# Optimization experiments

Hardware: AMD Instinct MI355X
Metric: run time of the kernel (lower is better)

The kernel has to match this reference:

```python
import jax, jax.numpy as jnp
import numpy as np

FFT_LEN = 256
WIN_LEN = 768
FRM_LEN = 128
PPF_TAP = WIN_LEN // FFT_LEN  # 6
SCALE = -256.0
GROUP_DELAY = 648  # module uses group_delay = -648
B, C, S, T = 8, 2, FFT_LEN // 2 + 1, 4096


def _make_lpf(win_len):
    # firwin(win_len, 0.5, window='hann', scale=False) equivalent
    n = np.arange(win_len, dtype=np.float64)
    w = 0.5 - 0.5 * np.cos(2.0 * np.pi * n / (win_len - 1))
    h = w * np.sinc(0.5 * (n - (win_len - 1) / 2.0))
    return jnp.asarray(h, dtype=jnp.float32)


def setup_inputs() -> dict:
    key = jax.random.key(0)
    k1, k2 = jax.random.split(key)
    spectrum_real = jax.random.normal(k1, (B, C, S, T), dtype=jnp.float32)
    spectrum_imag = jax.random.normal(k2, (B, C, S, T), dtype=jnp.float32)
    lpf_coef = _make_lpf(WIN_LEN)
    return {"spectrum_real": spectrum_real, "spectrum_imag": spectrum_imag, "lpf_coef": lpf_coef}


def reference(spectrum_real, spectrum_imag, lpf_coef):
    # spectrum: (B, C, S, T) complex; per-frame irfft over subbands
    spec = jnp.swapaxes(spectrum_real + 1j * spectrum_imag, -1, -2)  # (B,C,T,S)
    fftout = jnp.fft.irfft(spec, n=FFT_LEN, axis=-1)                 # (B,C,T,FFT_LEN)
    rev = fftout[..., ::-1]                                          # comp_in[fft_len-j-1]
    v = jnp.tile(rev, (1, 1, 1, PPF_TAP)) * lpf_coef                 # (B,C,T,WIN_LEN)
    b, c, t, _ = v.shape
    num_samples = t * FRM_LEN
    # overlap-add: frame t contributes v[t] at offset t*FRM_LEN (shifting buffer recurrence)
    idx = jnp.arange(t)[:, None] * FRM_LEN + jnp.arange(WIN_LEN)[None, :]  # (T, WIN_LEN)
    y = jnp.zeros((b, c, num_samples + WIN_LEN), dtype=v.dtype)
    y = y.at[..., idx].add(v)[..., :num_samples]
    y = y * (FRM_LEN * SCALE)
    # circular shift by group delay, then trim the wrapped tail
    y = jnp.roll(y, -GROUP_DELAY, axis=-1)[..., :-GROUP_DELAY]
    return y
```

## Files before the change

kernel.cpp:

```cpp
#include <hip/hip_runtime.h>
#include <hip/hip_bf16.h>
#include <math.h>

#define NBINS   129
#define NFFT    256
#define WINL    768
#define TFRAMES 4096
#define OUTL    523640
#define NPAIRS  (OUTL / 2)
#define SHIFT   648
#define WSEG    26
#define CHUNK   (WSEG * 128)
#define NCHUNK  ((OUTL + CHUNK - 1) / CHUNK)
#define FF      32

#define KDIM    288
#define KROW    296
#define GROW    268
#define WBYTES  (16 * 9 * 64 * 16)
#define GBYTES  ((size_t)16 * TFRAMES * 256 * 2)
#define NSTG    17

typedef __attribute__((ext_vector_type(8))) short bf16x8;
typedef __attribute__((ext_vector_type(4))) float f32x4;

static __device__ __forceinline__ ushort f2bf(float x) {
    union { float f; unsigned u; } v; v.f = x;
    unsigned r = v.u + 0x7FFFu + ((v.u >> 16) & 1u);
    return (ushort)(r >> 16);
}

__global__ void build_w_kernel(ushort* __restrict__ wp)
{
    const int gid  = blockIdx.x * 256 + threadIdx.x;
    const int lane = gid & 63;
    const int mtks = gid >> 6;
    const int ks   = mtks % 9;
    const int mt   = mtks / 9;
    const int m    = mt * 16 + (lane & 15);
    const int kb   = ks * 32 + ((lane >> 4) << 3);

    ushort o[8];
    #pragma unroll
    for (int e = 0; e < 8; ++e) {
        const int kap = kb + e;
        float val = 0.f;
        if (kap < 258) {
            const int k = kap >> 1;
            float s, c;
            sincospif((float)(k * (m + 1)) * (1.0f / 128.0f), &s, &c);
            if (kap & 1)  val = (k >= 1 && k <= 127) ? s * (2.0f / 256.0f) : 0.f;
            else          val = (k == 0 || k == 128) ? c * (1.0f / 256.0f)
                                                     : c * (2.0f / 256.0f);
        }
        o[e] = f2bf(val);
    }
    int4 pk;
    pk.x = o[0] | (o[1] << 16); pk.y = o[2] | (o[3] << 16);
    pk.z = o[4] | (o[5] << 16); pk.w = o[6] | (o[7] << 16);
    ((int4*)wp)[gid] = pk;
}

__global__ __launch_bounds__(256, 6)
void pfb_dft_kernel(const float* __restrict__ gre, const float* __restrict__ gim,
                    const ushort* __restrict__ wp, ushort* __restrict__ Gg)
{
    __shared__ ushort s_Bu[FF * KROW];

    const int t0  = blockIdx.x * FF;
    const int bc  = blockIdx.y;
    const int tid = threadIdx.x;
    const size_t specBase = (size_t)bc * NBINS * TFRAMES;

    float vr[NSTG], vi[NSTG];
    #pragma unroll
    for (int r = 0; r < NSTG; ++r) {
        const int idx = tid + r * 256;
        float a = 0.f, b = 0.f;
        if (idx < NBINS * FF) {
            const int k = idx >> 5, f = idx & 31;
            const size_t g = specBase + (size_t)k * TFRAMES + (size_t)(t0 + f);
            a = gre[g]; b = gim[g];
        }
        vr[r] = a; vi[r] = b;
    }
    #pragma unroll
    for (int r = 0; r < NSTG; ++r) {
        const int idx = tid + r * 256;
        if (idx < NBINS * FF) {
            const int k = idx >> 5, f = idx & 31;
            __hip_bfloat162 p = __float22bfloat162_rn(make_float2(vr[r], vi[r]));
            *(__hip_bfloat162*)&s_Bu[f * KROW + 2 * k] = p;
        }
    }
    for (int idx = tid; idx < FF * (KROW - 258); idx += 256) {
        const int f = idx / (KROW - 258), r = idx - f * (KROW - 258);
        s_Bu[f * KROW + 258 + r] = 0;
    }
    __syncthreads();

    const int lane = tid & 63;
    const int wid  = tid >> 6;
    const int brow = lane & 15;
    const int kgrp = (lane >> 4) << 3;

    f32x4 acc[4][2];
    #pragma unroll
    for (int mi = 0; mi < 4; ++mi)
        #pragma unroll
        for (int nt = 0; nt < 2; ++nt)
            acc[mi][nt] = (f32x4){0.f, 0.f, 0.f, 0.f};

    const ushort* wbase0 = wp + ((size_t)(wid * 4) * 9 * 64 + (size_t)lane) * 8;
    #pragma unroll
    for (int ks = 0; ks < 9; ++ks) {
        const bf16x8 b0 = *(const bf16x8*)&s_Bu[brow * KROW + ks * 32 + kgrp];
        const bf16x8 b1 = *(const bf16x8*)&s_Bu[(16 + brow) * KROW + ks * 32 + kgrp];
        #pragma unroll
        for (int mi = 0; mi < 4; ++mi) {
            const bf16x8 aw = *(const bf16x8*)(wbase0 + mi * 4608 + ks * 512);
            acc[mi][0] = __builtin_amdgcn_mfma_f32_16x16x32_bf16(aw, b0, acc[mi][0], 0, 0, 0);
            acc[mi][1] = __builtin_amdgcn_mfma_f32_16x16x32_bf16(aw, b1, acc[mi][1], 0, 0, 0);
        }
    }

    ushort* gout = Gg + ((size_t)bc * TFRAMES + t0) * NFFT;
    #pragma unroll
    for (int mi = 0; mi < 4; ++mi) {
        const int m0 = (wid * 4 + mi) * 16 + ((lane >> 4) << 2);
        #pragma unroll
        for (int nt = 0; nt < 2; ++nt) {
            const int f = nt * 16 + brow;
            __hip_bfloat162 lo = __float22bfloat162_rn(make_float2(acc[mi][nt].x, acc[mi][nt].y));
            __hip_bfloat162 hi = __float22bfloat162_rn(make_float2(acc[mi][nt].z, acc[mi][nt].w));
            uint2 pk; pk.x = *(unsigned*)&lo; pk.y = *(unsigned*)&hi;
            *(uint2*)&gout[f * NFFT + m0] = pk;
        }
    }
}

__global__ __launch_bounds__(256, 8)
void pfb_oa_kernel(const ushort* __restrict__ Gg, const float* __restrict__ glpf,
                   float* __restrict__ out)
{
    const int tid = threadIdx.x;
    const int bc  = blockIdx.y;
    const int g0  = blockIdx.x * 1024 + tid;

    const int b = (2 * g0 + SHIFT) & 127;
    float2 lw[6];
    #pragma unroll
    for (int p = 0; p < 6; ++p) lw[p] = *(const float2*)&glpf[(p << 7) + b];

    const ushort* Gb = Gg + (size_t)bc * TFRAMES * NFFT;
    const size_t outBase = (size_t)bc * OUTL;

    #pragma unroll
    for (int j = 0; j < 4; ++j) {
        const int g = g0 + j * 256;
        int a = (2 * g + SHIFT) >> 7;
        if (a > TFRAMES - 1) a = TFRAMES - 1;
        float sx = 0.f, sy = 0.f;
        #pragma unroll
        for (int p = 0; p < 6; ++p) {
            const unsigned pr = *(const unsigned*)&Gb[(size_t)(a - p) * NFFT + b + ((p & 1) << 7)];
            union { unsigned u; float f; } glo, ghi;
            glo.u = pr << 16;
            ghi.u = pr & 0xFFFF0000u;
            sx += lw[p].x * glo.f;
            sy += lw[p].y * ghi.f;
        }
        if (g < NPAIRS) {
            float2 o; o.x = sx * (-32768.0f); o.y = sy * (-32768.0f);
            *(float2*)&out[outBase + 2 * g] = o;
        }
    }
}

__global__ __launch_bounds__(256, 4)
void pfb_mfma_kernel(const float* __restrict__ gre, const float* __restrict__ gim,
                     const float* __restrict__ glpf, const ushort* __restrict__ wp,
                     float* __restrict__ out)
{
    __shared__ ushort s_bufu[FF * KROW];
    __shared__ float  s_lpf[WINL];
    ushort* s_Bu = s_bufu;
    ushort (*s_G)[GROW] = (ushort (*)[GROW])s_bufu;

    const int q   = blockIdx.x;
    const int bc  = blockIdx.y;
    const int tid = threadIdx.x;
    const int t0  = WSEG * q;
    const size_t specBase = (size_t)bc * NBINS * TFRAMES;

    for (int idx = tid; idx < WINL; idx += 256) s_lpf[idx] = glpf[idx];

    float vr[NSTG], vi[NSTG];
    #pragma unroll
    for (int r = 0; r < NSTG; ++r) {
        const int idx = tid + r * 256;
        const int k = idx >> 5, f = idx & 31;
        const int t = t0 + f;
        const bool ok = (idx < NBINS * FF) && (t < TFRAMES);
        float a = 0.f, bb = 0.f;
        if (ok) {
            const size_t g = specBase + (size_t)k * TFRAMES + (size_t)t;
            a = gre[g]; bb = gim[g];
        }
        vr[r] = a; vi[r] = bb;
    }
    #pragma unroll
    for (int r = 0; r < NSTG; ++r) {
        const int idx = tid + r * 256;
        if (idx < NBINS * FF) {
            const int k = idx >> 5, f = idx & 31;
            __hip_bfloat162 p = __float22bfloat162_rn(make_float2(vr[r], vi[r]));
            *(__hip_bfloat162*)&s_Bu[f * KROW + 2 * k] = p;
        }
    }
    for (int idx = tid; idx < FF * (KROW - 258); idx += 256) {
        const int f = idx / (KROW - 258), r = idx - f * (KROW - 258);
        s_Bu[f * KROW + 258 + r] = 0;
    }
    __syncthreads();

    const int lane = tid & 63;
    const int wid  = tid >> 6;
    const int brow = lane & 15;
    const int kgrp = (lane >> 4) << 3;

    bf16x8 bfrag[2][9];
    #pragma unroll
    for (int nt = 0; nt < 2; ++nt)
        #pragma unroll
        for (int ks = 0; ks < 9; ++ks)
            bfrag[nt][ks] = *(const bf16x8*)&s_Bu[(nt * 16 + brow) * KROW + ks * 32 + kgrp];

    f32x4 acc[4][2];
    #pragma unroll
    for (int mi = 0; mi < 4; ++mi)
        #pragma unroll
        for (int nt = 0; nt < 2; ++nt)
            acc[mi][nt] = (f32x4){0.f, 0.f, 0.f, 0.f};

    #pragma unroll 1
    for (int mi = 0; mi < 4; ++mi) {
        const ushort* wbase = wp + ((size_t)((wid * 4 + mi) * 9) * 64 + lane) * 8;
        #pragma unroll
        for (int ks = 0; ks < 9; ++ks) {
            const bf16x8 aw = *(const bf16x8*)(wbase + ks * 512);
            acc[mi][0] = __builtin_amdgcn_mfma_f32_16x16x32_bf16(aw, bfrag[0][ks], acc[mi][0], 0, 0, 0);
            acc[mi][1] = __builtin_amdgcn_mfma_f32_16x16x32_bf16(aw, bfrag[1][ks], acc[mi][1], 0, 0, 0);
        }
    }
    __syncthreads();

    #pragma unroll
    for (int mi = 0; mi < 4; ++mi) {
        const int m0 = (wid * 4 + mi) * 16 + ((lane >> 4) << 2);
        #pragma unroll
        for (int nt = 0; nt < 2; ++nt) {
            const int f = nt * 16 + brow;
            __hip_bfloat162 lo = __float22bfloat162_rn(make_float2(acc[mi][nt].x, acc[mi][nt].y));
            __hip_bfloat162 hi = __float22bfloat162_rn(make_float2(acc[mi][nt].z, acc[mi][nt].w));
            uint2 pk; pk.x = *(unsigned*)&lo; pk.y = *(unsigned*)&hi;
            *(uint2*)&s_G[f][m0] = pk;
        }
    }
    __syncthreads();

    const size_t outBase = (size_t)bc * OUTL;
    const int i0 = q * CHUNK;
    #pragma unroll 1
    for (int r = 0; r < 13; ++r) {
        const int i = i0 + r * 256 + tid;
        const int s = i + SHIFT;
        const int tlo = (s - 640) >> 7;
        int thi = s >> 7;
        if (thi > t0 + FF - 1) thi = t0 + FF - 1;
        if (thi > TFRAMES - 1) thi = TFRAMES - 1;
        float sum = 0.f;
        #pragma unroll
        for (int u = 0; u < 6; ++u) {
            const int t  = tlo + u;
            int jj = s - (t << 7);
            if (jj < 0) jj = 0;
            const float w = s_lpf[jj];
            union { unsigned u_; float f; } g;
            g.u_ = ((unsigned)s_G[t - t0][jj & 255]) << 16;
            sum += (t <= thi) ? w * g.f : 0.f;
        }
        if (i < OUTL) out[outBase + i] = sum * (-32768.0f);
    }
}

extern "C" void kernel_launch(void* const* d_in, const int* in_sizes, int n_in,
                              void* d_out, int out_size, void* d_ws, size_t ws_size,
                              hipStream_t stream)
{
    const float* gre  = (const float*)d_in[0];
    const float* gim  = (const float*)d_in[1];
    const float* glpf = (const float*)d_in[2];
    float* out = (float*)d_out;

    if (ws_size >= (size_t)WBYTES + GBYTES) {
        ushort* wp = (ushort*)d_ws;
        ushort* Gg = (ushort*)((char*)d_ws + WBYTES);
        build_w_kernel<<<36, 256, 0, stream>>>(wp);
        dim3 gridA(TFRAMES / FF, 16);
        pfb_dft_kernel<<<gridA, 256, 0, stream>>>(gre, gim, wp, Gg);
        dim3 gridB((NPAIRS + 1023) / 1024, 16);
        pfb_oa_kernel<<<gridB, 256, 0, stream>>>(Gg, glpf, out);
    } else if (ws_size >= (size_t)WBYTES) {
        ushort* wp = (ushort*)d_ws;
        build_w_kernel<<<36, 256, 0, stream>>>(wp);
        dim3 grid(NCHUNK, 16);
        pfb_mfma_kernel<<<grid, 256, 0, stream>>>(gre, gim, glpf, wp, out);
    }
}
```

Before: 56.36 us.

## Process four frame tiles per DFT block with double-buffered LDS prefetch

Each DFT block now handles four consecutive 32-frame tiles instead of one. The next tile's spectrum is prefetched into registers while the current tile's MFMA work runs, and then written into an alternate LDS buffer. The goal is to overlap global-load latency with matrix compute and amortize per-block setup. In exchange the grid is four times smaller (512 blocks), there are more registers and twice the LDS, and launch bounds drop to 4 waves.

```diff
diff --git a/kernel.cpp b/kernel.cpp
--- a/kernel.cpp
+++ b/kernel.cpp
@@ -13,6 +13,7 @@
 #define CHUNK   (WSEG * 128)
 #define NCHUNK  ((OUTL + CHUNK - 1) / CHUNK)
 #define FF      32
+#define TPB     4
 
 #define KDIM    288
 #define KROW    296
@@ -61,81 +62,101 @@
     ((int4*)wp)[gid] = pk;
 }
 
-__global__ __launch_bounds__(256, 6)
+__global__ __launch_bounds__(256, 4)
 void pfb_dft_kernel(const float* __restrict__ gre, const float* __restrict__ gim,
                     const ushort* __restrict__ wp, ushort* __restrict__ Gg)
 {
-    __shared__ ushort s_Bu[FF * KROW];
-
-    const int t0  = blockIdx.x * FF;
-    const int bc  = blockIdx.y;
-    const int tid = threadIdx.x;
+    __shared__ ushort s_Bu[2][FF * KROW];
+
+    const int tbase = blockIdx.x * TPB * FF;
+    const int bc    = blockIdx.y;
+    const int tid   = threadIdx.x;
     const size_t specBase = (size_t)bc * NBINS * TFRAMES;
-
-    float vr[NSTG], vi[NSTG];
-    #pragma unroll
-    for (int r = 0; r < NSTG; ++r) {
-        const int idx = tid + r * 256;
-        float a = 0.f, b = 0.f;
-        if (idx < NBINS * FF) {
-            const int k = idx >> 5, f = idx & 31;
-            const size_t g = specBase + (size_t)k * TFRAMES + (size_t)(t0 + f);
-            a = gre[g]; b = gim[g];
-        }
-        vr[r] = a; vi[r] = b;
-    }
-    #pragma unroll
-    for (int r = 0; r < NSTG; ++r) {
-        const int idx = tid + r * 256;
-        if (idx < NBINS * FF) {
-            const int k = idx >> 5, f = idx & 31;
-            __hip_bfloat162 p = __float22bfloat162_rn(make_float2(vr[r], vi[r]));
-            *(__hip_bfloat162*)&s_Bu[f * KROW + 2 * k] = p;
-        }
-    }
-    for (int idx = tid; idx < FF * (KROW - 258); idx += 256) {
-        const int f = idx / (KROW - 258), r = idx - f * (KROW - 258);
-        s_Bu[f * KROW + 258 + r] = 0;
-    }
-    __syncthreads();
 
     const int lane = tid & 63;
     const int wid  = tid >> 6;
     const int brow = lane & 15;
     const int kgrp = (lane >> 4) << 3;
-
-    f32x4 acc[4][2];
-    #pragma unroll
-    for (int mi = 0; mi < 4; ++mi)
-        #pragma unroll
-        for (int nt = 0; nt < 2; ++nt)
-            acc[mi][nt] = (f32x4){0.f, 0.f, 0.f, 0.f};
-
     const ushort* wbase0 = wp + ((size_t)(wid * 4) * 9 * 64 + (size_t)lane) * 8;
-    #pragma unroll
-    for (int ks = 0; ks < 9; ++ks) {
-        const bf16x8 b0 = *(const bf16x8*)&s_Bu[brow * KROW + ks * 32 + kgrp];
-        const bf16x8 b1 = *(const bf16x8*)&s_Bu[(16 + brow) * KROW + ks * 32 + kgrp];
+
+    float vr[NSTG], vi[NSTG];
+
+    auto LOAD = [&](int tile) {
+        const int tt0 = tbase + tile * FF;
+        #pragma unroll
+        for (int r = 0; r < NSTG; ++r) {
+            const int idx = tid + r * 256;
+            float a = 0.f, b = 0.f;
+            if (idx < NBINS * FF) {
+                const int k = idx >> 5, f = idx & 31;
+                const size_t g = specBase + (size_t)k * TFRAMES + (size_t)(tt0 + f);
+                a = gre[g]; b = gim[g];
+            }
+            vr[r] = a; vi[r] = b;
+        }
+    };
+    auto WLDS = [&](int buf) {
+        #pragma unroll
+        for (int r = 0; r < NSTG; ++r) {
+            const int idx = tid + r * 256;
+            if (idx < NBINS * FF) {
+                const int k = idx >> 5, f = idx & 31;
+                __hip_bfloat162 p = __float22bfloat162_rn(make_float2(vr[r], vi[r]));
+                *(__hip_bfloat162*)&s_Bu[buf][f * KROW + 2 * k] = p;
+            }
+        }
+    };
+
+    for (int idx = tid; idx < 2 * FF * (KROW - 258); idx += 256) {
+        const int bu  = idx / (FF * (KROW - 258));
+        const int rem = idx - bu * (FF * (KROW - 258));
+        const int f = rem / (KROW - 258), r2 = rem - f * (KROW - 258);
+        s_Bu[bu][f * KROW + 258 + r2] = 0;
+    }
+    LOAD(0);
+    WLDS(0);
+
+    #pragma unroll
+    for (int i = 0; i < TPB; ++i) {
+        const int cur = i & 1;
+        __syncthreads();
+
+        if (i + 1 < TPB) LOAD(i + 1);
+
+        f32x4 acc[4][2];
+        #pragma unroll
+        for (int mi = 0; mi < 4; ++mi)
+            #pragma unroll
+            for (int nt = 0; nt < 2; ++nt)
+                acc[mi][nt] = (f32x4){0.f, 0.f, 0.f, 0.f};
+
+        #pragma unroll
+        for (int ks = 0; ks < 9; ++ks) {
+            const bf16x8 b0 = *(const bf16x8*)&s_Bu[cur][brow * KROW + ks * 32 + kgrp];
+            const bf16x8 b1 = *(const bf16x8*)&s_Bu[cur][(16 + brow) * KROW + ks * 32 + kgrp];
+            #pragma unroll
+            for (int mi = 0; mi < 4; ++mi) {
+                const bf16x8 aw = *(const bf16x8*)(wbase0 + mi * 4608 + ks * 512);
+                acc[mi][0] = __builtin_amdgcn_mfma_f32_16x16x32_bf16(aw, b0, acc[mi][0], 0, 0, 0);
+                acc[mi][1] = __builtin_amdgcn_mfma_f32_16x16x32_bf16(aw, b1, acc[mi][1], 0, 0, 0);
+            }
+        }
+
+        ushort* gout = Gg + ((size_t)bc * TFRAMES + tbase + i * FF) * NFFT;
         #pragma unroll
         for (int mi = 0; mi < 4; ++mi) {
-            const bf16x8 aw = *(const bf16x8*)(wbase0 + mi * 4608 + ks * 512);
-            acc[mi][0] = __builtin_amdgcn_mfma_f32_16x16x32_bf16(aw, b0, acc[mi][0], 0, 0, 0);
-            acc[mi][1] = __builtin_amdgcn_mfma_f32_16x16x32_bf16(aw, b1, acc[mi][1], 0, 0, 0);
-        }
-    }
-
-    ushort* gout = Gg + ((size_t)bc * TFRAMES + t0) * NFFT;
-    #pragma unroll
-    for (int mi = 0; mi < 4; ++mi) {
-        const int m0 = (wid * 4 + mi) * 16 + ((lane >> 4) << 2);
-        #pragma unroll
-        for (int nt = 0; nt < 2; ++nt) {
-            const int f = nt * 16 + brow;
-            __hip_bfloat162 lo = __float22bfloat162_rn(make_float2(acc[mi][nt].x, acc[mi][nt].y));
-            __hip_bfloat162 hi = __float22bfloat162_rn(make_float2(acc[mi][nt].z, acc[mi][nt].w));
-            uint2 pk; pk.x = *(unsigned*)&lo; pk.y = *(unsigned*)&hi;
-            *(uint2*)&gout[f * NFFT + m0] = pk;
-        }
+            const int m0 = (wid * 4 + mi) * 16 + ((lane >> 4) << 2);
+            #pragma unroll
+            for (int nt = 0; nt < 2; ++nt) {
+                const int f = nt * 16 + brow;
+                __hip_bfloat162 lo = __float22bfloat162_rn(make_float2(acc[mi][nt].x, acc[mi][nt].y));
+                __hip_bfloat162 hi = __float22bfloat162_rn(make_float2(acc[mi][nt].z, acc[mi][nt].w));
+                uint2 pk; pk.x = *(unsigned*)&lo; pk.y = *(unsigned*)&hi;
+                *(uint2*)&gout[f * NFFT + m0] = pk;
+            }
+        }
+
+        if (i + 1 < TPB) WLDS(cur ^ 1);
     }
 }
 
@@ -307,7 +328,7 @@
         ushort* wp = (ushort*)d_ws;
         ushort* Gg = (ushort*)((char*)d_ws + WBYTES);
         build_w_kernel<<<36, 256, 0, stream>>>(wp);
-        dim3 gridA(TFRAMES / FF, 16);
+        dim3 gridA(TFRAMES / (FF * TPB), 16);
         pfb_dft_kernel<<<gridA, 256, 0, stream>>>(gre, gim, wp, Gg);
         dim3 gridB((NPAIRS + 1023) / 1024, 16);
         pfb_oa_kernel<<<gridB, 256, 0, stream>>>(Gg, glpf, out);
```

Result: slower. 113.4 us (+101.2%).
